# Optimization experiments

Hardware: AMD Instinct MI355X
Metric: run time of the kernel (lower is better)

Reference implementation:

```python
import jax, jax.numpy as jnp
import numpy as np

B, S, HID = 2, 2048, 2048
NH, NOPE, ROPE = 16, 128, 64
HD = NOPE + ROPE          # 192
VHD = 128
KVR, QR = 512, 1536
FFN = 5632
THETA = 10000.0
EPS = 1e-6


def rmsnorm(x, w, eps=EPS):
    xf = x.astype(jnp.float32)
    rms = jnp.sqrt(jnp.mean(xf * xf, axis=-1, keepdims=True) + eps)
    return (xf / rms).astype(x.dtype) * w


def apply_rope(x, cos, sin):
    # x: (..., rope_dim); half-split rotation convention
    half = x.shape[-1] // 2
    x1, x2 = x[..., :half], x[..., half:]
    return jnp.concatenate([x1 * cos - x2 * sin, x2 * cos + x1 * sin], axis=-1)


def rope_tables(seq_len, dim, theta=THETA):
    inv_freq = 1.0 / (theta ** (jnp.arange(0, dim, 2, dtype=jnp.float32) / dim))
    t = jnp.arange(seq_len, dtype=jnp.float32)
    freqs = jnp.outer(t, inv_freq)           # (S, dim/2)
    return jnp.cos(freqs), jnp.sin(freqs)


def setup_inputs():
    key = jax.random.key(0)
    ks = jax.random.split(key, 10)
    def w(k, shape, fan_in):
        return jax.random.normal(k, shape, dtype=jnp.float32) * (fan_in ** -0.5)
    return {
        'x': jax.random.normal(ks[0], (B, S, HID), dtype=jnp.float32),
        'attn_norm_w': jnp.ones((HID,), jnp.float32),
        'wq_down': w(ks[1], (HID, QR), HID),
        'wq_up': w(ks[2], (QR, NH * HD), QR),
        'wkv_down': w(ks[3], (HID, KVR + ROPE), HID),
        'kv_norm_w': jnp.ones((KVR,), jnp.float32),
        'wkv_up': w(ks[4], (KVR, NH * (NOPE + VHD)), KVR),
        'wout': w(ks[5], (NH * VHD, HID), NH * VHD),
        'ffn_norm_w': jnp.ones((HID,), jnp.float32),
        'w_gate': w(ks[6], (HID, FFN), HID),
        'w_up': w(ks[7], (HID, FFN), HID),
        'w_down': w(ks[8], (FFN, HID), FFN),
    }


def reference(x, attn_norm_w, wq_down, wq_up, wkv_down, kv_norm_w, wkv_up, wout,
              ffn_norm_w, w_gate, w_up, w_down):
    scale = 1.0 / np.sqrt(HD)
    # --- attention sub-block ---
    h = rmsnorm(x, attn_norm_w)
    q = (h @ wq_down) @ wq_up                       # (B,S,NH*HD)
    q = q.reshape(B, S, NH, HD)
    q_nope, q_rope = q[..., :NOPE], q[..., NOPE:]
    kv_full = h @ wkv_down                          # (B,S,KVR+ROPE)
    kv_c, k_rope = kv_full[..., :KVR], kv_full[..., KVR:]
    kv_c = rmsnorm(kv_c, kv_norm_w)
    kv_exp = (kv_c @ wkv_up).reshape(B, S, NH, NOPE + VHD)
    k_nope, v = kv_exp[..., :NOPE], kv_exp[..., NOPE:]

    cos, sin = rope_tables(S, ROPE)                 # (S, ROPE/2)
    cos4, sin4 = cos[None, :, None, :], sin[None, :, None, :]
    q_rope = apply_rope(q_rope, cos4, sin4)         # (B,S,NH,ROPE)
    k_rope = apply_rope(k_rope[:, :, None, :], cos4, sin4)  # (B,S,1,ROPE)
    k_rope = jnp.broadcast_to(k_rope, (B, S, NH, ROPE))

    q_full = jnp.concatenate([q_nope, q_rope], axis=-1)     # (B,S,NH,HD)
    k = jnp.concatenate([k_nope, k_rope], axis=-1)          # (B,S,NH,HD)

    scores = jnp.einsum('bqhd,bkhd->bhqk', q_full, k) * scale
    causal = jnp.tril(jnp.ones((S, S), dtype=bool))
    scores = jnp.where(causal[None, None], scores, jnp.finfo(scores.dtype).min)
    probs = jax.nn.softmax(scores, axis=-1)
    attn = jnp.einsum('bhqk,bkhd->bqhd', probs, v).reshape(B, S, NH * VHD)
    x = x + attn @ wout

    # --- SwiGLU MLP sub-block ---
    h2 = rmsnorm(x, ffn_norm_w)
    ffn = (jax.nn.silu(h2 @ w_gate) * (h2 @ w_up)) @ w_down
    return x + ffn
```

## Files before the change

kernel.cpp:

```cpp
#include <hip/hip_runtime.h>
#include <hip/hip_bf16.h>


using bf16x8 = __attribute__((ext_vector_type(8))) short;
using f32x4  = __attribute__((ext_vector_type(4))) float;

#define GLOBAL_AS __attribute__((address_space(1)))
#define LDS_AS    __attribute__((address_space(3)))
#define MFMA16(a, b, c) __builtin_amdgcn_mfma_f32_16x16x32_bf16((a), (b), (c), 0, 0, 0)

static constexpr int Sc = 2048;

__device__ __forceinline__ void gload16(const void* g, void* l) {
  __builtin_amdgcn_global_load_lds((const GLOBAL_AS unsigned int*)g,
                                   (LDS_AS unsigned int*)l, 16, 0, 0);
}
__device__ __forceinline__ float bf2f(unsigned short u) {
  union { float f; unsigned int i; } x; x.i = ((unsigned int)u) << 16; return x.f;
}
__device__ __forceinline__ unsigned short f2bf(float f) {
  union { float f; unsigned int i; } x; x.f = f;
  unsigned int i = x.i;
  return (unsigned short)((i + 0x7fffu + ((i >> 16) & 1u)) >> 16);
}
__device__ __forceinline__ int swz4(int r) { return ((r >> 2) & 3) ^ (r & 3); }

__global__ void fill_k(float* out, float v, int n) {
  int i = blockIdx.x * 256 + threadIdx.x;
  if (i < n) out[i] = v;
}

__global__ __launch_bounds__(256) void wtrans(const float* __restrict__ W,
                                              unsigned short* __restrict__ WT,
                                              int K, int N) {
  __shared__ float t[64][33];
  const int n0 = blockIdx.x * 32, k0 = blockIdx.y * 64;
  const int tx = threadIdx.x & 31, ty = threadIdx.x >> 5;
#pragma unroll
  for (int i = 0; i < 8; ++i) {
    int k = k0 + ty + i * 8;
    int n = n0 + tx;
    t[ty + i * 8][tx] = (n < N) ? W[(size_t)k * N + n] : 0.0f;
  }
  __syncthreads();
#pragma unroll
  for (int i = 0; i < 4; ++i) {
    int nl = ty + i * 8;
    int kp = tx;
    unsigned int lo = f2bf(t[kp * 2][nl]);
    unsigned int hi = f2bf(t[kp * 2 + 1][nl]);
    *(unsigned int*)(WT + (size_t)(n0 + nl) * K + k0 + kp * 2) = lo | (hi << 16);
  }
}

__global__ void rope_tab(float* __restrict__ cosT, float* __restrict__ sinT) {
  int i = blockIdx.x * 256 + threadIdx.x;
  if (i >= Sc * 32) return;
  int s = i >> 5, j = i & 31;
  float inv = powf(10000.0f, -(float)j / 32.0f);
  float a = (float)s * inv;
  cosT[i] = cosf(a);
  sinT[i] = sinf(a);
}

__global__ __launch_bounds__(256) void rmsnorm_k(const float* __restrict__ in,
                                                 const float* __restrict__ w,
                                                 unsigned short* __restrict__ out,
                                                 int D, int istride, int ostride) {
  const int row = blockIdx.x;
  const float* x = in + (size_t)row * istride;
  float ss = 0.f;
  for (int c = threadIdx.x * 4; c < D; c += 1024) {
    const float4 v = *(const float4*)(x + c);
    ss += v.x * v.x + v.y * v.y + v.z * v.z + v.w * v.w;
  }
#pragma unroll
  for (int off = 1; off < 64; off <<= 1) ss += __shfl_xor(ss, off);
  __shared__ float part[4];
  if ((threadIdx.x & 63) == 0) part[threadIdx.x >> 6] = ss;
  __syncthreads();
  float tot = part[0] + part[1] + part[2] + part[3];
  float r = rsqrtf(tot / (float)D + 1e-6f);
  for (int c = threadIdx.x * 4; c < D; c += 1024) {
    const float4 v = *(const float4*)(x + c);
    ushort4 o;
    o.x = f2bf(v.x * r * w[c + 0]);
    o.y = f2bf(v.y * r * w[c + 1]);
    o.z = f2bf(v.z * r * w[c + 2]);
    o.w = f2bf(v.w * r * w[c + 3]);
    *(ushort4*)(out + (size_t)row * ostride + c) = o;
  }
}

enum { EPI_BF16 = 0, EPI_F32 = 1, EPI_ADDF32 = 2, EPI_SILU = 3 };

template <int BMW, int EPI>
__global__ __launch_bounds__(512, 2) void gemm_big(const unsigned short* __restrict__ A,
                                                   const unsigned short* __restrict__ BT,
                                                   void* __restrict__ Cp,
                                                   const float* __restrict__ resid,
                                                   const unsigned short* __restrict__ other,
                                                   int M, int N, int K) {
  constexpr int BM = 128 * BMW;
  constexpr int AL = 2 * BMW;
  constexpr int MF = 4 * BMW;
  __shared__ unsigned short ldsA[2][BM * 64];
  __shared__ unsigned short ldsB[2][256 * 64];

  const int tid = threadIdx.x;
  const int w = tid >> 6, lane = tid & 63;
  const int rl = lane & 15, gh = lane >> 4;
  const int wm = w >> 2, wn = w & 3;

  const int nwg = gridDim.x;
  const int orig = blockIdx.x;
  const int qq = nwg >> 3, rr = nwg & 7;
  const int xcd = orig & 7, lidx = orig >> 3;
  const int fswz = (xcd < rr ? xcd * (qq + 1) : rr * (qq + 1) + (xcd - rr) * qq) + lidx;
  const int MT = M / BM;
  const int m0 = (fswz % MT) * BM;
  const int n0 = (fswz / MT) * 256;

  const unsigned short* srcA[AL];
#pragma unroll
  for (int i = 0; i < AL; ++i) {
    int G = i * 512 + tid, r = G >> 3, sl = (G & 7) ^ (r & 7);
    srcA[i] = A + (size_t)(m0 + r) * K + sl * 8;
  }
  const unsigned short* srcB[4];
#pragma unroll
  for (int i = 0; i < 4; ++i) {
    int G = i * 512 + tid, r = G >> 3, sl = (G & 7) ^ (r & 7);
    srcB[i] = BT + (size_t)(n0 + r) * K + sl * 8;
  }

  auto STAGE = [&](int kt, int p) {
    const int ko = kt * 64;
#pragma unroll
    for (int i = 0; i < AL; ++i)
      gload16(srcA[i] + ko, &ldsA[p][(i * 512 + w * 64) * 8]);
#pragma unroll
    for (int i = 0; i < 4; ++i)
      gload16(srcB[i] + ko, &ldsB[p][(i * 512 + w * 64) * 8]);
  };

  f32x4 acc[MF][4] = {};
  const int nk = K >> 6;

  STAGE(0, 0);
  STAGE(1, 1);
  if constexpr (BMW == 2) asm volatile("s_waitcnt vmcnt(8)" ::: "memory");
  else                    asm volatile("s_waitcnt vmcnt(6)" ::: "memory");
  __builtin_amdgcn_s_barrier();
  __builtin_amdgcn_sched_barrier(0);

  for (int kt = 0; kt < nk; ++kt) {
    const int cur = kt & 1;
    const unsigned short* lA = &ldsA[cur][0];
    const unsigned short* lB = &ldsB[cur][0];
    bf16x8 a[MF][2], b[4][2];
#pragma unroll
    for (int mf = 0; mf < MF; ++mf)
#pragma unroll
      for (int ks = 0; ks < 2; ++ks) {
        const int row = wm * (64 * BMW) + mf * 16 + rl;
        a[mf][ks] = *(const bf16x8*)&lA[row * 64 + (((ks << 2) + gh) ^ (row & 7)) * 8];
      }
#pragma unroll
    for (int nf = 0; nf < 4; ++nf)
#pragma unroll
      for (int ks = 0; ks < 2; ++ks) {
        const int row = wn * 64 + nf * 16 + rl;
        b[nf][ks] = *(const bf16x8*)&lB[row * 64 + (((ks << 2) + gh) ^ (row & 7)) * 8];
      }
    asm volatile("s_waitcnt lgkmcnt(0)" ::: "memory");
    __builtin_amdgcn_sched_barrier(0);
    __builtin_amdgcn_s_barrier();
    __builtin_amdgcn_sched_barrier(0);
    STAGE((kt + 2 < nk) ? kt + 2 : kt, cur);
    __builtin_amdgcn_s_setprio(1);
#pragma unroll
    for (int ks = 0; ks < 2; ++ks)
#pragma unroll
      for (int mf = 0; mf < MF; ++mf)
#pragma unroll
        for (int nf = 0; nf < 4; ++nf)
          acc[mf][nf] = MFMA16(a[mf][ks], b[nf][ks], acc[mf][nf]);
    __builtin_amdgcn_s_setprio(0);
    __builtin_amdgcn_sched_barrier(0);
    if constexpr (BMW == 2) asm volatile("s_waitcnt vmcnt(8)" ::: "memory");
    else                    asm volatile("s_waitcnt vmcnt(6)" ::: "memory");
    __builtin_amdgcn_s_barrier();
    __builtin_amdgcn_sched_barrier(0);
  }

#pragma unroll
  for (int mf = 0; mf < MF; ++mf) {
#pragma unroll
    for (int nf = 0; nf < 4; ++nf) {
#pragma unroll
      for (int rg = 0; rg < 4; ++rg) {
        const int row = m0 + wm * (64 * BMW) + mf * 16 + gh * 4 + rg;
        const int col = n0 + wn * 64 + nf * 16 + rl;
        const size_t idx = (size_t)row * N + col;
        const float v = acc[mf][nf][rg];
        if constexpr (EPI == EPI_BF16) {
          ((unsigned short*)Cp)[idx] = f2bf(v);
        } else if constexpr (EPI == EPI_F32) {
          ((float*)Cp)[idx] = v;
        } else if constexpr (EPI == EPI_ADDF32) {
          ((float*)Cp)[idx] = v + resid[idx];
        } else {
          float gv = bf2f(other[idx]);
          float sg = gv / (1.f + __expf(-gv));
          ((unsigned short*)Cp)[idx] = f2bf(sg * v);
        }
      }
    }
  }
}

template <int EPI>
__global__ __launch_bounds__(256) void gemm_bt(const unsigned short* __restrict__ A,
                                               const unsigned short* __restrict__ BT,
                                               void* __restrict__ Cp,
                                               const float* __restrict__ resid,
                                               const unsigned short* __restrict__ other,
                                               int M, int N, int K) {
  __shared__ unsigned short ldsA[2][128 * 32];
  __shared__ unsigned short ldsB[2][128 * 32];
  const int tid = threadIdx.x;
  const int w = tid >> 6, lane = tid & 63;
  const int nwg = gridDim.x;
  const int orig = blockIdx.x;
  const int qq = nwg >> 3, rr = nwg & 7;
  const int xcd = orig & 7, lidx = orig >> 3;
  const int fswz = (xcd < rr ? xcd * (qq + 1) : rr * (qq + 1) + (xcd - rr) * qq) + lidx;
  const int m0 = (fswz & 31) * 128;
  const int n0 = (fswz >> 5) * 128;

  const int wm = (w >> 1) * 64, wn = (w & 1) * 64;
  const int rl = lane & 15, gsel = lane >> 4;

  const int p0 = w * 64 + lane;
  const int p1 = p0 + 256;
  const int r0 = p0 >> 2, r1 = p1 >> 2;
  const int g0 = (p0 & 3) ^ swz4(r0), g1 = (p1 & 3) ^ swz4(r1);
  const unsigned short* gA0 = A + (size_t)(m0 + r0) * K + g0 * 8;
  const unsigned short* gA1 = A + (size_t)(m0 + r1) * K + g1 * 8;
  const unsigned short* gB0 = BT + (size_t)(n0 + r0) * K + g0 * 8;
  const unsigned short* gB1 = BT + (size_t)(n0 + r1) * K + g1 * 8;
  const int dA0 = (w * 64) * 8, dA1 = dA0 + 2048;

  int aoff[4], boff[4];
#pragma unroll
  for (int i = 0; i < 4; ++i) {
    int ra = wm + i * 16 + rl;
    aoff[i] = ra * 32 + (gsel ^ swz4(ra)) * 8;
    int rb = wn + i * 16 + rl;
    boff[i] = rb * 32 + (gsel ^ swz4(rb)) * 8;
  }

  auto STAGE = [&](int kt, int p) {
    const int ko = kt * 32;
    gload16(gA0 + ko, &ldsA[p][dA0]);
    gload16(gA1 + ko, &ldsA[p][dA1]);
    gload16(gB0 + ko, &ldsB[p][dA0]);
    gload16(gB1 + ko, &ldsB[p][dA1]);
  };

  f32x4 acc[4][4] = {};
  const int nk = K >> 5;

  STAGE(0, 0);
  STAGE(1, 1);
  for (int kt = 0; kt < nk; ++kt) {
    asm volatile("s_waitcnt vmcnt(4)" ::: "memory");
    __builtin_amdgcn_s_barrier();
    __builtin_amdgcn_sched_barrier(0);
    const unsigned short* lA = &ldsA[kt & 1][0];
    const unsigned short* lB = &ldsB[kt & 1][0];
    bf16x8 a[4], b[4];
#pragma unroll
    for (int i = 0; i < 4; ++i) a[i] = *(const bf16x8*)&lA[aoff[i]];
#pragma unroll
    for (int i = 0; i < 4; ++i) b[i] = *(const bf16x8*)&lB[boff[i]];
    __builtin_amdgcn_s_setprio(1);
#pragma unroll
    for (int i = 0; i < 4; ++i)
#pragma unroll
      for (int j = 0; j < 4; ++j) acc[i][j] = MFMA16(a[i], b[j], acc[i][j]);
    __builtin_amdgcn_s_setprio(0);
    __builtin_amdgcn_sched_barrier(0);
    __builtin_amdgcn_s_barrier();
    const int nxt = (kt + 2 < nk) ? kt + 2 : nk - 1;
    STAGE(nxt, kt & 1);
  }

#pragma unroll
  for (int i = 0; i < 4; ++i) {
#pragma unroll
    for (int j = 0; j < 4; ++j) {
#pragma unroll
      for (int rg = 0; rg < 4; ++rg) {
        const int row = m0 + wm + i * 16 + gsel * 4 + rg;
        const int col = n0 + wn + j * 16 + rl;
        const size_t idx = (size_t)row * N + col;
        const float v = acc[i][j][rg];
        if constexpr (EPI == EPI_BF16) {
          ((unsigned short*)Cp)[idx] = f2bf(v);
        } else if constexpr (EPI == EPI_F32) {
          ((float*)Cp)[idx] = v;
        } else if constexpr (EPI == EPI_ADDF32) {
          ((float*)Cp)[idx] = v + resid[idx];
        } else {
          float gv = bf2f(other[idx]);
          float sg = gv / (1.f + __expf(-gv));
          ((unsigned short*)Cp)[idx] = f2bf(sg * v);
        }
      }
    }
  }
}

__global__ __launch_bounds__(256) void repack_q(const unsigned short* __restrict__ q,
                                                const float* __restrict__ cosT,
                                                const float* __restrict__ sinT,
                                                unsigned short* __restrict__ Qc) {
  const int row = blockIdx.x;
  const int b = row >> 11, s = row & 2047;
  const float scale = 0.07216878364870322f;
  const unsigned short* qr = q + (size_t)row * 3072;
  for (int i = threadIdx.x; i < 3072; i += 256) {
    int h = i / 192, d = i - h * 192;
    float v;
    if (d < 128) {
      v = bf2f(qr[h * 192 + d]);
    } else {
      int j = d - 128;
      int jj = j & 31;
      float x1 = bf2f(qr[h * 192 + 128 + jj]);
      float x2 = bf2f(qr[h * 192 + 160 + jj]);
      float c = cosT[s * 32 + jj], sn = sinT[s * 32 + jj];
      v = (j < 32) ? (x1 * c - x2 * sn) : (x2 * c + x1 * sn);
    }
    Qc[((size_t)(b * 16 + h) * Sc + s) * 192 + d] = f2bf(v * scale);
  }
}

__global__ __launch_bounds__(256) void repack_kv(const unsigned short* __restrict__ kvex,
                                                 const float* __restrict__ kvf,
                                                 const float* __restrict__ cosT,
                                                 const float* __restrict__ sinT,
                                                 unsigned short* __restrict__ Kc,
                                                 unsigned short* __restrict__ VT) {
  __shared__ unsigned short vt_lds[32][136];
  const int bid = blockIdx.x;
  const int st = bid & 63;
  const int h = (bid >> 6) & 15;
  const int b = bid >> 10;
  const int s0 = st * 32;
  const int tid = threadIdx.x;
  const size_t KcBase = (size_t)(b * 16 + h) * Sc;
  for (int i = tid; i < 32 * 32; i += 256) {
    int r = i >> 5, g = i & 31;
    uint4 vdat = *(const uint4*)(kvex + (size_t)(b * Sc + s0 + r) * 4096 + h * 256 + g * 8);
    if (g < 16) {
      *(uint4*)(Kc + (KcBase + s0 + r) * 192 + g * 8) = vdat;
    } else {
      *(uint4*)(&vt_lds[r][(g - 16) * 8]) = vdat;
    }
  }
  for (int i = tid; i < 32 * 64; i += 256) {
    int r = i >> 6, d = i & 63;
    int s = s0 + r;
    int jj = d & 31;
    const float* kvrow = kvf + (size_t)(b * Sc + s) * 640;
    float x1 = kvrow[512 + jj], x2 = kvrow[544 + jj];
    float c = cosT[s * 32 + jj], sn = sinT[s * 32 + jj];
    float v = (d < 32) ? (x1 * c - x2 * sn) : (x2 * c + x1 * sn);
    Kc[(KcBase + s) * 192 + 128 + d] = f2bf(v);
  }
  __syncthreads();
  const int f = tid >> 1, sh = (tid & 1) * 16;
  unsigned int vals[8];
#pragma unroll
  for (int k2 = 0; k2 < 8; ++k2) {
    unsigned int lo = vt_lds[sh + 2 * k2][f];
    unsigned int hi = vt_lds[sh + 2 * k2 + 1][f];
    vals[k2] = lo | (hi << 16);
  }
  unsigned short* dst = VT + ((size_t)(b * 16 + h) * 128 + f) * Sc + s0 + sh;
  ((uint4*)dst)[0] = make_uint4(vals[0], vals[1], vals[2], vals[3]);
  ((uint4*)dst)[1] = make_uint4(vals[4], vals[5], vals[6], vals[7]);
}

__global__ __launch_bounds__(512) void attn_k(const unsigned short* __restrict__ Qc,
                                              const unsigned short* __restrict__ Kc,
                                              const unsigned short* __restrict__ VT,
                                              unsigned short* __restrict__ Ob) {
  __shared__ unsigned short lds_k[2][64 * 192];
  __shared__ unsigned short lds_v[2][128 * 64];
  __shared__ __align__(16) unsigned short p_lds[8][16 * 72];
  const int tid = threadIdx.x, w = tid >> 6, lane = tid & 63;
  const int rl = lane & 15, gh = lane >> 4;
  const int bidx = blockIdx.x;
  const int bh = bidx & 31;
  const int qt = 15 - (bidx >> 5);
  const unsigned short* Qh = Qc + (size_t)bh * Sc * 192;
  const unsigned short* Kh = Kc + (size_t)bh * Sc * 192;
  const unsigned short* Vh = VT + (size_t)bh * 128 * Sc;
  const int qr0 = qt * 128 + w * 16;

  bf16x8 qf[6];
#pragma unroll
  for (int kk = 0; kk < 6; ++kk)
    qf[kk] = *(const bf16x8*)(Qh + (size_t)(qr0 + rl) * 192 + kk * 32 + gh * 8);

  f32x4 o[8] = {};
  float mrun[4] = {-1e30f, -1e30f, -1e30f, -1e30f};
  float srun[4] = {0.f, 0.f, 0.f, 0.f};

  int kr[3], kg[3];
#pragma unroll
  for (int j = 0; j < 3; ++j) {
    int G = j * 512 + tid;
    int r = G / 24, gq = G - r * 24;
    kr[j] = r;
    kg[j] = (gq & ~7) | ((gq & 7) ^ (r & 7));
  }
  int vr[2], vg[2];
#pragma unroll
  for (int j = 0; j < 2; ++j) {
    int G = j * 512 + tid;
    int r = G >> 3;
    vr[j] = r;
    vg[j] = (G & 7) ^ (r & 7);
  }

  auto STAGE = [&](int t, int b) {
    const int k0 = t * 64;
#pragma unroll
    for (int j = 0; j < 3; ++j)
      gload16(Kh + (size_t)(k0 + kr[j]) * 192 + kg[j] * 8,
              &lds_k[b][(j * 512 + w * 64) * 8]);
#pragma unroll
    for (int j = 0; j < 2; ++j)
      gload16(Vh + (size_t)vr[j] * Sc + k0 + vg[j] * 8,
              &lds_v[b][(j * 512 + w * 64) * 8]);
  };

  STAGE(0, 0);
  asm volatile("s_waitcnt vmcnt(0)" ::: "memory");
  __builtin_amdgcn_s_barrier();
  __builtin_amdgcn_sched_barrier(0);

  const int nt = 2 * qt + 2;
  int cur = 0;
  for (int t = 0; t < nt; ++t) {
    if (t + 1 < nt) STAGE(t + 1, cur ^ 1);
    const int k0 = t * 64;
    if (k0 <= qr0 + 15) {
      const unsigned short* lk = lds_k[cur];
      const unsigned short* lv = lds_v[cur];
      f32x4 s[4] = {};
      __builtin_amdgcn_s_setprio(1);
#pragma unroll
      for (int kk = 0; kk < 6; ++kk) {
        const int gq = kk * 4 + gh;
#pragma unroll
        for (int ks = 0; ks < 4; ++ks) {
          const int krow = ks * 16 + rl;
          const int ph = (gq & ~7) | ((gq & 7) ^ (krow & 7));
          bf16x8 kf = *(const bf16x8*)&lk[krow * 192 + ph * 8];
          s[ks] = MFMA16(qf[kk], kf, s[ks]);
        }
      }
      __builtin_amdgcn_s_setprio(0);
      if (k0 + 63 > qr0) {
#pragma unroll
        for (int ks = 0; ks < 4; ++ks)
#pragma unroll
          for (int rg = 0; rg < 4; ++rg) {
            int qrow = qr0 + gh * 4 + rg;
            if (k0 + ks * 16 + rl > qrow) s[ks][rg] = -1e30f;
          }
      }
      float tmax[4];
#pragma unroll
      for (int rg = 0; rg < 4; ++rg) {
        float v = fmaxf(fmaxf(s[0][rg], s[1][rg]), fmaxf(s[2][rg], s[3][rg]));
        v = fmaxf(v, __shfl_xor(v, 1));
        v = fmaxf(v, __shfl_xor(v, 2));
        v = fmaxf(v, __shfl_xor(v, 4));
        v = fmaxf(v, __shfl_xor(v, 8));
        tmax[rg] = v;
      }
      int need = !(tmax[0] <= mrun[0] + 8.f && tmax[1] <= mrun[1] + 8.f &&
                   tmax[2] <= mrun[2] + 8.f && tmax[3] <= mrun[3] + 8.f);
      if (__any(need)) {
        float al[4];
#pragma unroll
        for (int rg = 0; rg < 4; ++rg) {
          float mn = fmaxf(mrun[rg], tmax[rg]);
          al[rg] = __expf(mrun[rg] - mn);
          mrun[rg] = mn;
          srun[rg] *= al[rg];
        }
#pragma unroll
        for (int i = 0; i < 8; ++i)
#pragma unroll
          for (int rg = 0; rg < 4; ++rg) o[i][rg] *= al[rg];
      }
      unsigned short* pw = p_lds[w];
#pragma unroll
      for (int ks = 0; ks < 4; ++ks)
#pragma unroll
        for (int rg = 0; rg < 4; ++rg) {
          float p = __expf(s[ks][rg] - mrun[rg]);
          srun[rg] += p;
          pw[(gh * 4 + rg) * 72 + ks * 16 + rl] = f2bf(p);
        }
      bf16x8 pa0 = *(const bf16x8*)&pw[rl * 72 + 0 * 32 + gh * 8];
      bf16x8 pa1 = *(const bf16x8*)&pw[rl * 72 + 1 * 32 + gh * 8];
      __builtin_amdgcn_s_setprio(1);
#pragma unroll
      for (int vf = 0; vf < 8; ++vf) {
        const int row = vf * 16 + rl;
        bf16x8 v0 = *(const bf16x8*)&lv[row * 64 + ((0 * 4 + gh) ^ (row & 7)) * 8];
        o[vf] = MFMA16(pa0, v0, o[vf]);
        bf16x8 v1 = *(const bf16x8*)&lv[row * 64 + ((1 * 4 + gh) ^ (row & 7)) * 8];
        o[vf] = MFMA16(pa1, v1, o[vf]);
      }
      __builtin_amdgcn_s_setprio(0);
    }
    asm volatile("s_waitcnt vmcnt(0)" ::: "memory");
    __builtin_amdgcn_s_barrier();
    __builtin_amdgcn_sched_barrier(0);
    cur ^= 1;
  }
  float rd[4];
#pragma unroll
  for (int rg = 0; rg < 4; ++rg) {
    float rs = srun[rg];
    rs += __shfl_xor(rs, 1);
    rs += __shfl_xor(rs, 2);
    rs += __shfl_xor(rs, 4);
    rs += __shfl_xor(rs, 8);
    rd[rg] = 1.f / rs;
  }
  const int b = bh >> 4, hh = bh & 15;
#pragma unroll
  for (int vf = 0; vf < 8; ++vf) {
#pragma unroll
    for (int rg = 0; rg < 4; ++rg) {
      int srow = qr0 + gh * 4 + rg;
      int col = hh * 128 + vf * 16 + rl;
      Ob[((size_t)(b * Sc) + srow) * 2048 + col] = f2bf(o[vf][rg] * rd[rg]);
    }
  }
}

extern "C" void kernel_launch(void* const* d_in, const int* in_sizes, int n_in,
                              void* d_out, int out_size, void* d_ws, size_t ws_size,
                              hipStream_t stream) {
  (void)in_sizes; (void)n_in;
  const float* x    = (const float*)d_in[0];
  const float* anw  = (const float*)d_in[1];
  const float* wqd  = (const float*)d_in[2];
  const float* wqu  = (const float*)d_in[3];
  const float* wkvd = (const float*)d_in[4];
  const float* kvnw = (const float*)d_in[5];
  const float* wkvu = (const float*)d_in[6];
  const float* wout = (const float*)d_in[7];
  const float* fnw  = (const float*)d_in[8];
  const float* wg   = (const float*)d_in[9];
  const float* wu   = (const float*)d_in[10];
  const float* wd   = (const float*)d_in[11];
  float* out = (float*)d_out;

  char* ws = (char*)d_ws;
  size_t off = 0;
  auto alloc = [&](size_t bytes) -> char* {
    char* p = ws + off;
    off += (bytes + 255) & ~(size_t)255;
    return p;
  };
  unsigned short* wslot = (unsigned short*)alloc(5632ull * 2048 * 2);
  float* cosT           = (float*)alloc(2048ull * 32 * 4);
  float* sinT           = (float*)alloc(2048ull * 32 * 4);
  unsigned short* hbuf  = (unsigned short*)alloc(4096ull * 2048 * 2);
  char* arena           = alloc(4096ull * 1536 * 2 + 4096ull * 3072 * 2);
  float* kvf            = (float*)alloc(4096ull * 640 * 4);
  unsigned short* kvn   = (unsigned short*)alloc(4096ull * 512 * 2);
  unsigned short* Qc    = (unsigned short*)alloc(32ull * 2048 * 192 * 2);
  unsigned short* Kc    = (unsigned short*)alloc(32ull * 2048 * 192 * 2);
  unsigned short* VTb   = (unsigned short*)alloc(32ull * 128 * 2048 * 2);
  const size_t NEED = off;

  if (ws_size < NEED) {
    fill_k<<<dim3((out_size + 255) / 256), dim3(256), 0, stream>>>(
        out, (float)(ws_size >> 20), out_size);
    return;
  }

  unsigned short* qd    = (unsigned short*)arena;
  unsigned short* q     = (unsigned short*)(arena + 4096ull * 1536 * 2);
  unsigned short* kvex  = (unsigned short*)arena;
  unsigned short* h     = hbuf;
  unsigned short* attnb = hbuf;
  unsigned short* h2    = hbuf;
  unsigned short* gbuf  = Qc;
  float* x2             = out;

  dim3 blk(256), blk512(512);
  rope_tab<<<dim3(256), blk, 0, stream>>>(cosT, sinT);
  rmsnorm_k<<<dim3(4096), blk, 0, stream>>>(x, anw, h, 2048, 2048, 2048);

  wtrans<<<dim3(48, 32), blk, 0, stream>>>(wqd, wslot, 2048, 1536);
  gemm_big<1, EPI_BF16><<<dim3(32 * 6), blk512, 0, stream>>>(h, wslot, qd, nullptr, nullptr, 4096, 1536, 2048);
  wtrans<<<dim3(96, 24), blk, 0, stream>>>(wqu, wslot, 1536, 3072);
  gemm_big<2, EPI_BF16><<<dim3(16 * 12), blk512, 0, stream>>>(qd, wslot, q, nullptr, nullptr, 4096, 3072, 1536);
  repack_q<<<dim3(4096), blk, 0, stream>>>(q, cosT, sinT, Qc);

  wtrans<<<dim3(20, 32), blk, 0, stream>>>(wkvd, wslot, 2048, 576);
  gemm_bt<EPI_F32><<<dim3(5 * 32), blk, 0, stream>>>(h, wslot, kvf, nullptr, nullptr, 4096, 640, 2048);
  rmsnorm_k<<<dim3(4096), blk, 0, stream>>>(kvf, kvnw, kvn, 512, 640, 512);
  wtrans<<<dim3(128, 8), blk, 0, stream>>>(wkvu, wslot, 512, 4096);
  gemm_big<2, EPI_BF16><<<dim3(16 * 16), blk512, 0, stream>>>(kvn, wslot, kvex, nullptr, nullptr, 4096, 4096, 512);
  repack_kv<<<dim3(2048), blk, 0, stream>>>(kvex, kvf, cosT, sinT, Kc, VTb);

  attn_k<<<dim3(512), blk512, 0, stream>>>(Qc, Kc, VTb, attnb);
  wtrans<<<dim3(64, 32), blk, 0, stream>>>(wout, wslot, 2048, 2048);
  gemm_big<1, EPI_ADDF32><<<dim3(32 * 8), blk512, 0, stream>>>(attnb, wslot, x2, x, nullptr, 4096, 2048, 2048);

  rmsnorm_k<<<dim3(4096), blk, 0, stream>>>(x2, fnw, h2, 2048, 2048, 2048);
  wtrans<<<dim3(176, 32), blk, 0, stream>>>(wg, wslot, 2048, 5632);
  gemm_big<2, EPI_BF16><<<dim3(16 * 22), blk512, 0, stream>>>(h2, wslot, gbuf, nullptr, nullptr, 4096, 5632, 2048);
  wtrans<<<dim3(176, 32), blk, 0, stream>>>(wu, wslot, 2048, 5632);
  gemm_big<2, EPI_SILU><<<dim3(16 * 22), blk512, 0, stream>>>(h2, wslot, gbuf, nullptr, gbuf, 4096, 5632, 2048);
  wtrans<<<dim3(64, 88), blk, 0, stream>>>(wd, wslot, 5632, 2048);
  gemm_big<1, EPI_ADDF32><<<dim3(32 * 8), blk512, 0, stream>>>(gbuf, wslot, out, x2, nullptr, 4096, 2048, 5632);
}
```

Before: 796.6 us.

## Add 256x256 eight-phase pipelined GEMM kernel for large BF16 projections

Adds a new 256x256-tile GEMM that splits each 64-wide K step into two 32-wide halves. It interleaves global-to-LDS loads for the next tile with MFMA phases, using barriers, explicit waitcnts and setprio. Tiles are remapped by XCD so neighbouring workgroups share L2. It replaces gemm_big<2> for the q-up, kv-up, gate and up projections, aiming to hide load latency behind compute. In exchange it runs one workgroup per CU and has more barriers per K step.

After: 841.3 us. 1.06x slower.

```diff
diff --git a/kernel.cpp b/kernel.cpp
--- a/kernel.cpp
+++ b/kernel.cpp
@@ -93,6 +93,170 @@
 }
 
 enum { EPI_BF16 = 0, EPI_F32 = 1, EPI_ADDF32 = 2, EPI_SILU = 3 };
+
+__device__ __forceinline__ void epilogue_store(void* Cp, const float* resid,
+                                               const unsigned short* other,
+                                               size_t idx, float v, int EPI) {}
+
+template <int EPI>
+__global__ __launch_bounds__(512, 1) void gemm_8p(const unsigned short* __restrict__ A,
+                                                  const unsigned short* __restrict__ BT,
+                                                  void* __restrict__ Cp,
+                                                  const float* __restrict__ resid,
+                                                  const unsigned short* __restrict__ other,
+                                                  int M, int N, int K) {
+  __shared__ unsigned short ldsA[2][2][256 * 32];
+  __shared__ unsigned short ldsB[2][2][256 * 32];
+  const int tid = threadIdx.x;
+  const int w = tid >> 6, lane = tid & 63;
+  const int rl = lane & 15, gh = lane >> 4;
+  const int wm = w >> 2, wn = w & 3;
+
+  const int nwg = gridDim.x;
+  const int orig = blockIdx.x;
+  const int qq = nwg >> 3, rr = nwg & 7;
+  const int xcd = orig & 7, lidx = orig >> 3;
+  const int fswz = (xcd < rr ? xcd * (qq + 1) : rr * (qq + 1) + (xcd - rr) * qq) + lidx;
+  const int MT = M >> 8;
+  const int m0 = (fswz % MT) * 256;
+  const int n0 = (fswz / MT) * 256;
+
+  int srow[2], sgr[2];
+#pragma unroll
+  for (int j = 0; j < 2; ++j) {
+    int G = j * 512 + tid;
+    srow[j] = G >> 2;
+    sgr[j] = ((G & 3) - (srow[j] >> 1)) & 3;
+  }
+  const unsigned short* sA[2];
+  const unsigned short* sB[2];
+#pragma unroll
+  for (int j = 0; j < 2; ++j) {
+    sA[j] = A + (size_t)(m0 + srow[j]) * K + sgr[j] * 8;
+    sB[j] = BT + (size_t)(n0 + srow[j]) * K + sgr[j] * 8;
+  }
+
+  int aoff[8], boff[4];
+#pragma unroll
+  for (int mf = 0; mf < 8; ++mf) {
+    int R = wm * 128 + mf * 16 + rl;
+    aoff[mf] = R * 32 + ((gh + (R >> 1)) & 3) * 8;
+  }
+#pragma unroll
+  for (int nf = 0; nf < 4; ++nf) {
+    int R = wn * 64 + nf * 16 + rl;
+    boff[nf] = R * 32 + ((gh + (R >> 1)) & 3) * 8;
+  }
+
+  auto STA = [&](int kt, int kh, int p) {
+#pragma unroll
+    for (int j = 0; j < 2; ++j)
+      gload16(sA[j] + kt * 64 + kh * 32, &ldsA[p][kh][(j * 512 + w * 64) * 8]);
+  };
+  auto STB = [&](int kt, int kh, int p) {
+#pragma unroll
+    for (int j = 0; j < 2; ++j)
+      gload16(sB[j] + kt * 64 + kh * 32, &ldsB[p][kh][(j * 512 + w * 64) * 8]);
+  };
+
+  f32x4 acc[8][4] = {};
+  const int nk = K >> 6;
+
+  STA(0, 0, 0); STB(0, 0, 0); STA(0, 1, 0); STB(0, 1, 0);
+  asm volatile("s_waitcnt vmcnt(4)" ::: "memory");
+  __builtin_amdgcn_s_barrier();
+
+  for (int kt = 0; kt < nk; ++kt) {
+    const int cur = kt & 1, nx = cur ^ 1;
+    const int ktn = (kt + 1 < nk) ? kt + 1 : kt;
+    bf16x8 a[4], b[4];
+#pragma unroll
+    for (int i = 0; i < 4; ++i) a[i] = *(const bf16x8*)&ldsA[cur][0][aoff[i]];
+#pragma unroll
+    for (int i = 0; i < 4; ++i) b[i] = *(const bf16x8*)&ldsB[cur][0][boff[i]];
+    STA(ktn, 0, nx);
+    __builtin_amdgcn_s_barrier();
+    asm volatile("s_waitcnt lgkmcnt(0)" ::: "memory");
+    __builtin_amdgcn_sched_barrier(0);
+    __builtin_amdgcn_s_setprio(1);
+#pragma unroll
+    for (int i = 0; i < 4; ++i)
+#pragma unroll
+      for (int j = 0; j < 4; ++j) acc[i][j] = MFMA16(a[i], b[j], acc[i][j]);
+    __builtin_amdgcn_s_setprio(0);
+    asm volatile("s_waitcnt vmcnt(4)" ::: "memory");
+    __builtin_amdgcn_s_barrier();
+#pragma unroll
+    for (int i = 0; i < 4; ++i) a[i] = *(const bf16x8*)&ldsA[cur][0][aoff[4 + i]];
+    STB(ktn, 0, nx);
+    __builtin_amdgcn_s_barrier();
+    asm volatile("s_waitcnt lgkmcnt(0)" ::: "memory");
+    __builtin_amdgcn_sched_barrier(0);
+    __builtin_amdgcn_s_setprio(1);
+#pragma unroll
+    for (int i = 0; i < 4; ++i)
+#pragma unroll
+      for (int j = 0; j < 4; ++j) acc[4 + i][j] = MFMA16(a[i], b[j], acc[4 + i][j]);
+    __builtin_amdgcn_s_setprio(0);
+    asm volatile("s_waitcnt vmcnt(4)" ::: "memory");
+    __builtin_amdgcn_s_barrier();
+#pragma unroll
+    for (int i = 0; i < 4; ++i) a[i] = *(const bf16x8*)&ldsA[cur][1][aoff[i]];
+#pragma unroll
+    for (int i = 0; i < 4; ++i) b[i] = *(const bf16x8*)&ldsB[cur][1][boff[i]];
+    STA(ktn, 1, nx);
+    __builtin_amdgcn_s_barrier();
+    asm volatile("s_waitcnt lgkmcnt(0)" ::: "memory");
+    __builtin_amdgcn_sched_barrier(0);
+    __builtin_amdgcn_s_setprio(1);
+#pragma unroll
+    for (int i = 0; i < 4; ++i)
+#pragma unroll
+      for (int j = 0; j < 4; ++j) acc[i][j] = MFMA16(a[i], b[j], acc[i][j]);
+    __builtin_amdgcn_s_setprio(0);
+    asm volatile("s_waitcnt vmcnt(4)" ::: "memory");
+    __builtin_amdgcn_s_barrier();
+#pragma unroll
+    for (int i = 0; i < 4; ++i) a[i] = *(const bf16x8*)&ldsA[cur][1][aoff[4 + i]];
+    STB(ktn, 1, nx);
+    __builtin_amdgcn_s_barrier();
+    asm volatile("s_waitcnt lgkmcnt(0)" ::: "memory");
+    __builtin_amdgcn_sched_barrier(0);
+    __builtin_amdgcn_s_setprio(1);
+#pragma unroll
+    for (int i = 0; i < 4; ++i)
+#pragma unroll
+      for (int j = 0; j < 4; ++j) acc[4 + i][j] = MFMA16(a[i], b[j], acc[4 + i][j]);
+    __builtin_amdgcn_s_setprio(0);
+    asm volatile("s_waitcnt vmcnt(4)" ::: "memory");
+    __builtin_amdgcn_s_barrier();
+  }
+
+#pragma unroll
+  for (int mf = 0; mf < 8; ++mf) {
+#pragma unroll
+    for (int nf = 0; nf < 4; ++nf) {
+#pragma unroll
+      for (int rg = 0; rg < 4; ++rg) {
+        const int row = m0 + wm * 128 + mf * 16 + gh * 4 + rg;
+        const int col = n0 + wn * 64 + nf * 16 + rl;
+        const size_t idx = (size_t)row * N + col;
+        const float v = acc[mf][nf][rg];
+        if constexpr (EPI == EPI_BF16) {
+          ((unsigned short*)Cp)[idx] = f2bf(v);
+        } else if constexpr (EPI == EPI_F32) {
+          ((float*)Cp)[idx] = v;
+        } else if constexpr (EPI == EPI_ADDF32) {
+          ((float*)Cp)[idx] = v + resid[idx];
+        } else {
+          float gv = bf2f(other[idx]);
+          float sg = gv / (1.f + __expf(-gv));
+          ((unsigned short*)Cp)[idx] = f2bf(sg * v);
+        }
+      }
+    }
+  }
+}
 
 template <int BMW, int EPI>
 __global__ __launch_bounds__(512, 2) void gemm_big(const unsigned short* __restrict__ A,
@@ -620,14 +784,14 @@
   wtrans<<<dim3(48, 32), blk, 0, stream>>>(wqd, wslot, 2048, 1536);
   gemm_big<1, EPI_BF16><<<dim3(32 * 6), blk512, 0, stream>>>(h, wslot, qd, nullptr, nullptr, 4096, 1536, 2048);
   wtrans<<<dim3(96, 24), blk, 0, stream>>>(wqu, wslot, 1536, 3072);
-  gemm_big<2, EPI_BF16><<<dim3(16 * 12), blk512, 0, stream>>>(qd, wslot, q, nullptr, nullptr, 4096, 3072, 1536);
+  gemm_8p<EPI_BF16><<<dim3(16 * 12), blk512, 0, stream>>>(qd, wslot, q, nullptr, nullptr, 4096, 3072, 1536);
   repack_q<<<dim3(4096), blk, 0, stream>>>(q, cosT, sinT, Qc);
 
   wtrans<<<dim3(20, 32), blk, 0, stream>>>(wkvd, wslot, 2048, 576);
   gemm_bt<EPI_F32><<<dim3(5 * 32), blk, 0, stream>>>(h, wslot, kvf, nullptr, nullptr, 4096, 640, 2048);
   rmsnorm_k<<<dim3(4096), blk, 0, stream>>>(kvf, kvnw, kvn, 512, 640, 512);
   wtrans<<<dim3(128, 8), blk, 0, stream>>>(wkvu, wslot, 512, 4096);
-  gemm_big<2, EPI_BF16><<<dim3(16 * 16), blk512, 0, stream>>>(kvn, wslot, kvex, nullptr, nullptr, 4096, 4096, 512);
+  gemm_8p<EPI_BF16><<<dim3(16 * 16), blk512, 0, stream>>>(kvn, wslot, kvex, nullptr, nullptr, 4096, 4096, 512);
   repack_kv<<<dim3(2048), blk, 0, stream>>>(kvex, kvf, cosT, sinT, Kc, VTb);
 
   attn_k<<<dim3(512), blk512, 0, stream>>>(Qc, Kc, VTb, attnb);
@@ -636,9 +800,9 @@
 
   rmsnorm_k<<<dim3(4096), blk, 0, stream>>>(x2, fnw, h2, 2048, 2048, 2048);
   wtrans<<<dim3(176, 32), blk, 0, stream>>>(wg, wslot, 2048, 5632);
-  gemm_big<2, EPI_BF16><<<dim3(16 * 22), blk512, 0, stream>>>(h2, wslot, gbuf, nullptr, nullptr, 4096, 5632, 2048);
+  gemm_8p<EPI_BF16><<<dim3(16 * 22), blk512, 0, stream>>>(h2, wslot, gbuf, nullptr, nullptr, 4096, 5632, 2048);
   wtrans<<<dim3(176, 32), blk, 0, stream>>>(wu, wslot, 2048, 5632);
-  gemm_big<2, EPI_SILU><<<dim3(16 * 22), blk512, 0, stream>>>(h2, wslot, gbuf, nullptr, gbuf, 4096, 5632, 2048);
+  gemm_8p<EPI_SILU><<<dim3(16 * 22), blk512, 0, stream>>>(h2, wslot, gbuf, nullptr, gbuf, 4096, 5632, 2048);
   wtrans<<<dim3(64, 88), blk, 0, stream>>>(wd, wslot, 5632, 2048);
   gemm_big<1, EPI_ADDF32><<<dim3(32 * 8), blk512, 0, stream>>>(gbuf, wslot, out, x2, nullptr, 4096, 2048, 5632);
 }
```

## Vectorize weight transpose and use a 128x128 single-buffer GEMM for gate

Applied to the files above, without the earlier changes.

The weight transpose kernel now works on 64x64 tiles, reading with float4 loads and writing eight bf16 values per 16-byte store. This is meant to cut the memory-instruction overhead of converting the fp32 weights each call. The FFN gate projection moves to a new 256-thread, 128x128-tile GEMM with a single LDS buffer and XCD-aware block remapping, which gives more, smaller workgroups. The transpose drops its N bounds check, so the kv-down padding columns in the weight slot are no longer zeroed. That relies on the padded outputs never being read, and the single-buffered GEMM cannot overlap its loads with compute.

Measured after the change: 783.2 us. No clear change (-1.7%).

```diff
diff --git a/kernel.cpp b/kernel.cpp
--- a/kernel.cpp
+++ b/kernel.cpp
@@ -33,23 +33,27 @@
 __global__ __launch_bounds__(256) void wtrans(const float* __restrict__ W,
                                               unsigned short* __restrict__ WT,
                                               int K, int N) {
-  __shared__ float t[64][33];
-  const int n0 = blockIdx.x * 32, k0 = blockIdx.y * 64;
-  const int tx = threadIdx.x & 31, ty = threadIdx.x >> 5;
-#pragma unroll
-  for (int i = 0; i < 8; ++i) {
-    int k = k0 + ty + i * 8;
-    int n = n0 + tx;
-    t[ty + i * 8][tx] = (n < N) ? W[(size_t)k * N + n] : 0.0f;
+  __shared__ float t[64][65];
+  const int n0 = blockIdx.x * 64, k0 = blockIdx.y * 64;
+  const int tx = threadIdx.x & 15, ty = threadIdx.x >> 4;
+#pragma unroll
+  for (int i = 0; i < 4; ++i) {
+    int k = k0 + ty + i * 16;
+    const float4 v = *(const float4*)(W + (size_t)k * N + n0 + tx * 4);
+    t[ty + i * 16][tx * 4 + 0] = v.x;
+    t[ty + i * 16][tx * 4 + 1] = v.y;
+    t[ty + i * 16][tx * 4 + 2] = v.z;
+    t[ty + i * 16][tx * 4 + 3] = v.w;
   }
   __syncthreads();
-#pragma unroll
-  for (int i = 0; i < 4; ++i) {
-    int nl = ty + i * 8;
-    int kp = tx;
-    unsigned int lo = f2bf(t[kp * 2][nl]);
-    unsigned int hi = f2bf(t[kp * 2 + 1][nl]);
-    *(unsigned int*)(WT + (size_t)(n0 + nl) * K + k0 + kp * 2) = lo | (hi << 16);
+  const int kx = threadIdx.x & 7, ny = threadIdx.x >> 3;
+#pragma unroll
+  for (int i = 0; i < 2; ++i) {
+    int nl = ny + i * 32;
+    unsigned short u[8];
+#pragma unroll
+    for (int j = 0; j < 8; ++j) u[j] = f2bf(t[kx * 8 + j][nl]);
+    *(uint4*)(WT + (size_t)(n0 + nl) * K + k0 + kx * 8) = *(uint4*)u;
   }
 }
 
@@ -93,6 +97,114 @@
 }
 
 enum { EPI_BF16 = 0, EPI_F32 = 1, EPI_ADDF32 = 2, EPI_SILU = 3 };
+
+template <int EPI>
+__global__ __launch_bounds__(256) void gemm_sb1(const unsigned short* __restrict__ A,
+                                                const unsigned short* __restrict__ BT,
+                                                void* __restrict__ Cp,
+                                                const float* __restrict__ resid,
+                                                const unsigned short* __restrict__ other,
+                                                int M, int N, int K) {
+  __shared__ unsigned short ldsA[128 * 64];
+  __shared__ unsigned short ldsB[128 * 64];
+  const int tid = threadIdx.x;
+  const int w = tid >> 6, lane = tid & 63;
+  const int rl = lane & 15, gh = lane >> 4;
+  const int wm = (w >> 1) * 64, wn = (w & 1) * 64;
+
+  const int nwg = gridDim.x;
+  const int orig = blockIdx.x;
+  const int qq = nwg >> 3, rr = nwg & 7;
+  const int xcd = orig & 7, lidx = orig >> 3;
+  const int fswz = (xcd < rr ? xcd * (qq + 1) : rr * (qq + 1) + (xcd - rr) * qq) + lidx;
+  const int MT = M >> 7;
+  const int m0 = (fswz % MT) * 128;
+  const int n0 = (fswz / MT) * 128;
+
+  const unsigned short* sA[4];
+  const unsigned short* sB[4];
+#pragma unroll
+  for (int i = 0; i < 4; ++i) {
+    int G = i * 256 + tid, r = G >> 3, sl = (G & 7) ^ (r & 7);
+    sA[i] = A + (size_t)(m0 + r) * K + sl * 8;
+    sB[i] = BT + (size_t)(n0 + r) * K + sl * 8;
+  }
+  auto STAGE = [&](int kt) {
+    const int ko = kt * 64;
+#pragma unroll
+    for (int i = 0; i < 4; ++i) {
+      gload16(sA[i] + ko, &ldsA[(i * 256 + w * 64) * 8]);
+      gload16(sB[i] + ko, &ldsB[(i * 256 + w * 64) * 8]);
+    }
+  };
+
+  int aoff[4], boff[4];
+#pragma unroll
+  for (int i = 0; i < 4; ++i) {
+    aoff[i] = (wm + i * 16 + rl) * 64;
+    boff[i] = (wn + i * 16 + rl) * 64;
+  }
+
+  f32x4 acc[4][4] = {};
+  const int nk = K >> 6;
+
+  STAGE(0);
+  asm volatile("s_waitcnt vmcnt(0)" ::: "memory");
+  __builtin_amdgcn_s_barrier();
+
+  for (int kt = 0; kt < nk; ++kt) {
+    bf16x8 a[4][2], b[4][2];
+#pragma unroll
+    for (int i = 0; i < 4; ++i)
+#pragma unroll
+      for (int ks = 0; ks < 2; ++ks) {
+        const int ra = wm + i * 16 + rl;
+        a[i][ks] = *(const bf16x8*)&ldsA[aoff[i] + ((((ks << 2) + gh)) ^ (ra & 7)) * 8];
+        const int rb = wn + i * 16 + rl;
+        b[i][ks] = *(const bf16x8*)&ldsB[boff[i] + ((((ks << 2) + gh)) ^ (rb & 7)) * 8];
+      }
+    __builtin_amdgcn_s_setprio(1);
+#pragma unroll
+    for (int ks = 0; ks < 2; ++ks)
+#pragma unroll
+      for (int i = 0; i < 4; ++i)
+#pragma unroll
+        for (int j = 0; j < 4; ++j) acc[i][j] = MFMA16(a[i][ks], b[j][ks], acc[i][j]);
+    __builtin_amdgcn_s_setprio(0);
+    asm volatile("s_waitcnt lgkmcnt(0)" ::: "memory");
+    __builtin_amdgcn_sched_barrier(0);
+    __builtin_amdgcn_s_barrier();
+    STAGE((kt + 1 < nk) ? kt + 1 : nk - 1);
+    asm volatile("s_waitcnt vmcnt(0)" ::: "memory");
+    __builtin_amdgcn_sched_barrier(0);
+    __builtin_amdgcn_s_barrier();
+  }
+
+#pragma unroll
+  for (int i = 0; i < 4; ++i) {
+#pragma unroll
+    for (int j = 0; j < 4; ++j) {
+#pragma unroll
+      for (int rg = 0; rg < 4; ++rg) {
+        const int row = m0 + wm + i * 16 + gh * 4 + rg;
+        const int col = n0 + wn + j * 16 + rl;
+        const size_t idx = (size_t)row * N + col;
+        const float v = acc[i][j][rg];
+        if constexpr (EPI == EPI_BF16) {
+          ((unsigned short*)Cp)[idx] = f2bf(v);
+        } else if constexpr (EPI == EPI_F32) {
+          ((float*)Cp)[idx] = v;
+        } else if constexpr (EPI == EPI_ADDF32) {
+          ((float*)Cp)[idx] = v + resid[idx];
+        } else {
+          float gv = bf2f(other[idx]);
+          float sg = gv / (1.f + __expf(-gv));
+          ((unsigned short*)Cp)[idx] = f2bf(sg * v);
+        }
+      }
+    }
+  }
+}
 
 template <int BMW, int EPI>
 __global__ __launch_bounds__(512, 2) void gemm_big(const unsigned short* __restrict__ A,
@@ -617,28 +729,28 @@
   rope_tab<<<dim3(256), blk, 0, stream>>>(cosT, sinT);
   rmsnorm_k<<<dim3(4096), blk, 0, stream>>>(x, anw, h, 2048, 2048, 2048);
 
-  wtrans<<<dim3(48, 32), blk, 0, stream>>>(wqd, wslot, 2048, 1536);
+  wtrans<<<dim3(24, 32), blk, 0, stream>>>(wqd, wslot, 2048, 1536);
   gemm_big<1, EPI_BF16><<<dim3(32 * 6), blk512, 0, stream>>>(h, wslot, qd, nullptr, nullptr, 4096, 1536, 2048);
-  wtrans<<<dim3(96, 24), blk, 0, stream>>>(wqu, wslot, 1536, 3072);
+  wtrans<<<dim3(48, 24), blk, 0, stream>>>(wqu, wslot, 1536, 3072);
   gemm_big<2, EPI_BF16><<<dim3(16 * 12), blk512, 0, stream>>>(qd, wslot, q, nullptr, nullptr, 4096, 3072, 1536);
   repack_q<<<dim3(4096), blk, 0, stream>>>(q, cosT, sinT, Qc);
 
-  wtrans<<<dim3(20, 32), blk, 0, stream>>>(wkvd, wslot, 2048, 576);
+  wtrans<<<dim3(9, 32), blk, 0, stream>>>(wkvd, wslot, 2048, 576);
   gemm_bt<EPI_F32><<<dim3(5 * 32), blk, 0, stream>>>(h, wslot, kvf, nullptr, nullptr, 4096, 640, 2048);
   rmsnorm_k<<<dim3(4096), blk, 0, stream>>>(kvf, kvnw, kvn, 512, 640, 512);
-  wtrans<<<dim3(128, 8), blk, 0, stream>>>(wkvu, wslot, 512, 4096);
+  wtrans<<<dim3(64, 8), blk, 0, stream>>>(wkvu, wslot, 512, 4096);
   gemm_big<2, EPI_BF16><<<dim3(16 * 16), blk512, 0, stream>>>(kvn, wslot, kvex, nullptr, nullptr, 4096, 4096, 512);
   repack_kv<<<dim3(2048), blk, 0, stream>>>(kvex, kvf, cosT, sinT, Kc, VTb);
 
   attn_k<<<dim3(512), blk512, 0, stream>>>(Qc, Kc, VTb, attnb);
-  wtrans<<<dim3(64, 32), blk, 0, stream>>>(wout, wslot, 2048, 2048);
+  wtrans<<<dim3(32, 32), blk, 0, stream>>>(wout, wslot, 2048, 2048);
   gemm_big<1, EPI_ADDF32><<<dim3(32 * 8), blk512, 0, stream>>>(attnb, wslot, x2, x, nullptr, 4096, 2048, 2048);
 
   rmsnorm_k<<<dim3(4096), blk, 0, stream>>>(x2, fnw, h2, 2048, 2048, 2048);
-  wtrans<<<dim3(176, 32), blk, 0, stream>>>(wg, wslot, 2048, 5632);
-  gemm_big<2, EPI_BF16><<<dim3(16 * 22), blk512, 0, stream>>>(h2, wslot, gbuf, nullptr, nullptr, 4096, 5632, 2048);
-  wtrans<<<dim3(176, 32), blk, 0, stream>>>(wu, wslot, 2048, 5632);
+  wtrans<<<dim3(88, 32), blk, 0, stream>>>(wg, wslot, 2048, 5632);
+  gemm_sb1<EPI_BF16><<<dim3(32 * 44), blk, 0, stream>>>(h2, wslot, gbuf, nullptr, nullptr, 4096, 5632, 2048);
+  wtrans<<<dim3(88, 32), blk, 0, stream>>>(wu, wslot, 2048, 5632);
   gemm_big<2, EPI_SILU><<<dim3(16 * 22), blk512, 0, stream>>>(h2, wslot, gbuf, nullptr, gbuf, 4096, 5632, 2048);
-  wtrans<<<dim3(64, 88), blk, 0, stream>>>(wd, wslot, 5632, 2048);
+  wtrans<<<dim3(32, 88), blk, 0, stream>>>(wd, wslot, 5632, 2048);
   gemm_big<1, EPI_ADDF32><<<dim3(32 * 8), blk512, 0, stream>>>(gbuf, wslot, out, x2, nullptr, 4096, 2048, 5632);
 }
```
